# Performance work log

Hardware: AMD Instinct MI355X
Metric: run time of the kernel (lower is better)

## Reference

```python
import jax, jax.numpy as jnp
import numpy as np

TEMPERATURE = 0.07
NEG_RATIO = 1.0
ADJ_DENSITY = 0.002
SAMPLE_SEED = 42


def setup_inputs() -> dict:
    key = jax.random.key(0)
    k1, k2, k3 = jax.random.split(key, 3)
    I, E, D = 4096, 16384, 64
    item = jax.random.normal(k1, (I, D), dtype=jnp.float32)
    ent = jax.random.normal(k2, (E, D), dtype=jnp.float32)
    # sparse binary adjacency: ~33 positives per item on average
    adj = (jax.random.uniform(k3, (I, E)) < ADJ_DENSITY).astype(jnp.int32)
    return {"item_embeddings": item, "entity_embeddings": ent, "adj_matrix": adj}


def reference(item_embeddings, entity_embeddings, adj_matrix):
    # L2-normalize rows, cosine similarity / temperature
    it = item_embeddings / jnp.linalg.norm(item_embeddings, axis=1, keepdims=True)
    en = entity_embeddings / jnp.linalg.norm(entity_embeddings, axis=1, keepdims=True)
    sim = jnp.einsum('id,ed->ie', it, en) / TEMPERATURE  # [I, E]

    pos_mask = adj_matrix > 0                             # [I, E]
    neg_mask = ~pos_mask
    num_pos = pos_mask.sum(axis=1)                        # [I]
    num_neg = neg_mask.sum(axis=1)
    # num_negatives = min(int(num_pos * ratio), num_neg)  (per item)
    k = jnp.minimum(jnp.floor(num_pos.astype(jnp.float32) * NEG_RATIO).astype(jnp.int32), num_neg)

    # negative sampling without replacement: uniform keys, take k smallest among negatives
    u = jax.random.uniform(jax.random.key(SAMPLE_SEED), sim.shape)
    u = jnp.where(pos_mask, jnp.inf, u)                   # positives rank last
    rank = jnp.argsort(jnp.argsort(u, axis=1), axis=1)    # per-row rank of each entity
    samp = (rank < k[:, None]) & neg_mask                 # sampled negatives [I, E]

    valid = (num_pos > 0) & (k > 0)                       # items contributing pairs

    # stable per-item logsumexp over sampled negatives
    neg_logits = jnp.where(samp, sim, -jnp.inf)
    m = jnp.max(neg_logits, axis=1)                       # [I], -inf if no sampled negs
    m_safe = jnp.where(valid, m, 0.0)
    S = jnp.sum(jnp.where(samp, jnp.exp(sim - m_safe[:, None]), 0.0), axis=1)  # [I]

    # per positive pair: CE with pos as class 0 over [pos, sampled_negs]
    # loss = log(exp(pos) + sum exp(neg)) - pos, stabilized with pairwise max
    pm = jnp.maximum(sim, m_safe[:, None])
    loss_pair = jnp.log(jnp.exp(sim - pm) + S[:, None] * jnp.exp(m_safe[:, None] - pm)) + pm - sim

    pair_mask = pos_mask & valid[:, None]
    total = jnp.sum(jnp.where(pair_mask, loss_pair, 0.0))
    n_pairs = jnp.sum(jnp.where(valid, num_pos, 0))
    return jnp.where(n_pairs > 0, total / jnp.maximum(n_pairs, 1).astype(jnp.float32), 0.0)
```

## Files before the change

### kernel.cpp

```cpp
#include <hip/hip_runtime.h>
#include <math.h>


constexpr int D      = 64;
constexpr int PCAP   = 96;
constexpr int CCAP   = 192;
constexpr int SELCAP = 128;

typedef int int4v __attribute__((ext_vector_type(4)));

__device__ __forceinline__ void threefry2x32(unsigned x0, unsigned x1,
                                             unsigned& o0, unsigned& o1) {
  const unsigned ks0 = 0u;
  const unsigned ks1 = 42u;
  const unsigned ks2 = 0x1BD11BDAu ^ 0u ^ 42u;
  x0 += ks0; x1 += ks1;
#define TF_R(r) { x0 += x1; x1 = (x1 << (r)) | (x1 >> (32 - (r))); x1 ^= x0; }
  TF_R(13) TF_R(15) TF_R(26) TF_R(6)
  x0 += ks1; x1 += ks2 + 1u;
  TF_R(17) TF_R(29) TF_R(16) TF_R(24)
  x0 += ks2; x1 += ks0 + 2u;
  TF_R(13) TF_R(15) TF_R(26) TF_R(6)
  x0 += ks0; x1 += ks1 + 3u;
  TF_R(17) TF_R(29) TF_R(16) TF_R(24)
  x0 += ks1; x1 += ks2 + 4u;
  TF_R(13) TF_R(15) TF_R(26) TF_R(6)
  x0 += ks2; x1 += ks0 + 5u;
#undef TF_R
  o0 = x0; o1 = x1;
}

__device__ __forceinline__ float dot_sim(const float* __restrict__ ent, int e,
                                         const float* itemn) {
  const float4* er = (const float4*)(ent + ((size_t)e << 6));
  float dot = 0.f, ss = 0.f;
#pragma unroll
  for (int q = 0; q < 16; ++q) {
    float4 f = er[q];
    dot += itemn[4 * q + 0] * f.x + itemn[4 * q + 1] * f.y +
           itemn[4 * q + 2] * f.z + itemn[4 * q + 3] * f.w;
    ss += f.x * f.x + f.y * f.y + f.z * f.z + f.w * f.w;
  }
  return dot * (1.0f / sqrtf(ss));
}

__device__ __forceinline__ void wave_append(bool pred, int e,
                                            int* cnt, int* list, int cap) {
  unsigned long long m = __ballot(pred);
  if (m) {
    const int lane = threadIdx.x & 63;
    const int leader = __builtin_ctzll(m);
    int base = 0;
    if (lane == leader) base = atomicAdd(cnt, __popcll(m));
    base = __shfl(base, leader, 64);
    if (pred) {
      int s = base + __popcll(m & ((1ull << lane) - 1ull));
      if (s < cap) list[s] = e;
    }
  }
}

__device__ __forceinline__ void wave_append2(bool pred, int e, unsigned key,
                                             int* cnt, int* li, unsigned* lk,
                                             int cap) {
  unsigned long long m = __ballot(pred);
  if (m) {
    const int lane = threadIdx.x & 63;
    const int leader = __builtin_ctzll(m);
    int base = 0;
    if (lane == leader) base = atomicAdd(cnt, __popcll(m));
    base = __shfl(base, leader, 64);
    if (pred) {
      int s = base + __popcll(m & ((1ull << lane) - 1ull));
      if (s < cap) { li[s] = e; lk[s] = key; }
    }
  }
}

__device__ __forceinline__ float block_max(float v, float* wred, int t) {
#pragma unroll
  for (int off = 32; off; off >>= 1) v = fmaxf(v, __shfl_xor(v, off, 64));
  __syncthreads();
  if ((t & 63) == 0) wred[t >> 6] = v;
  __syncthreads();
  return fmaxf(fmaxf(wred[0], wred[1]), fmaxf(wred[2], wred[3]));
}

__device__ __forceinline__ float block_sum(float v, float* wred, int t) {
#pragma unroll
  for (int off = 32; off; off >>= 1) v += __shfl_xor(v, off, 64);
  __syncthreads();
  if ((t & 63) == 0) wred[t >> 6] = v;
  __syncthreads();
  return wred[0] + wred[1] + wred[2] + wred[3];
}

template <bool WSOUT>
__global__ __launch_bounds__(256) void infonce_mono(
    const float* __restrict__ item, const float* __restrict__ ent,
    const int* __restrict__ adj, int I, int E,
    float* __restrict__ loss, int* __restrict__ cnt,
    double* __restrict__ accum, int* __restrict__ paircnt) {
  const int t = threadIdx.x;
  const int halfI = I >> 1;
  const int iA = blockIdx.x;
  const int iB = iA + halfI;
  const unsigned HALF = (unsigned)halfI * (unsigned)E;
  const unsigned baseA = (unsigned)iA * (unsigned)E;

  __shared__ int s_pos[2][PCAP];
  __shared__ int s_ci[2][CCAP];
  __shared__ unsigned s_ck[2][CCAP];
  __shared__ int s_sel[SELCAP];
  __shared__ int s_hist[256];
  __shared__ float s_itemn[D];
  __shared__ float s_wred[4];
  __shared__ int s_np[2], s_nc[2];
  __shared__ int s_nsel, s_bbin, s_cbef, s_fnc;
  __shared__ float s_scale;

  if (t < 2) { s_np[t] = 0; s_nc[t] = 0; }
  __syncthreads();

  const int nvec = E >> 2;
  const int4v* adjA = (const int4v*)(adj + (size_t)iA * E);
  const int4v* adjB = (const int4v*)(adj + (size_t)iB * E);
  for (int v = t; v < nvec; v += 256) {
    int4v a4 = __builtin_nontemporal_load(&adjA[v]);
    int4v b4 = __builtin_nontemporal_load(&adjB[v]);
    const unsigned e0 = (unsigned)v * 4u;
    unsigned o0[4], o1[4];
#pragma unroll
    for (int c = 0; c < 4; ++c)
      threefry2x32(baseA + e0 + c, baseA + e0 + c + HALF, o0[c], o1[c]);
#pragma unroll
    for (int c = 0; c < 4; ++c) {
      const int e = (int)(e0 + c);
      const bool pa = (a4[c] > 0), pb = (b4[c] > 0);
      wave_append(pa, e, &s_np[0], s_pos[0], PCAP);
      wave_append(pb, e, &s_np[1], s_pos[1], PCAP);
      wave_append2(!pa && (o0[c] >> 24) == 0u, e, o0[c] >> 9,
                   &s_nc[0], s_ci[0], s_ck[0], CCAP);
      wave_append2(!pb && (o1[c] >> 24) == 0u, e, o1[c] >> 9,
                   &s_nc[1], s_ci[1], s_ck[1], CCAP);
    }
  }
  __syncthreads();

  for (int r2 = 0; r2 < 2; ++r2) {
    const int row = r2 ? iB : iA;
    const int npos = min(s_np[r2], PCAP);
    const int k = min(npos, E - npos);
    const bool valid = (npos > 0 && k > 0);
    float rowloss = 0.f;
    if (valid) {
      if (t == 0) s_nsel = 0;
      __syncthreads();
      int ncand = min(s_nc[r2], CCAP);
      int rneed = k;
      if (s_nc[r2] > CCAP || ncand < k) {
        s_hist[t] = 0;
        if (t == 0) s_fnc = 0;
        __syncthreads();
        const int* adjR = adj + (size_t)row * E;
        for (int e = t; e < E; e += 256) {
          if (adjR[e] > 0) continue;
          unsigned o0, o1;
          threefry2x32(baseA + (unsigned)e, baseA + (unsigned)e + HALF, o0, o1);
          atomicAdd(&s_hist[(r2 ? o1 : o0) >> 24], 1);
        }
        __syncthreads();
        if (t == 0) {
          int cum = 0, b = 0;
          while (b < 255 && cum + s_hist[b] < k) { cum += s_hist[b]; ++b; }
          s_bbin = b; s_cbef = cum;
        }
        __syncthreads();
        const int b = s_bbin;
        for (int e = t; e < E; e += 256) {
          bool neg = (adjR[e] <= 0);
          unsigned o0, o1, bits = 0xFFFFFFFFu;
          if (neg) {
            threefry2x32(baseA + (unsigned)e, baseA + (unsigned)e + HALF, o0, o1);
            bits = r2 ? o1 : o0;
          }
          int b8 = (int)(bits >> 24);
          wave_append(neg && b8 < b, e, &s_nsel, s_sel, SELCAP);
          wave_append2(neg && b8 == b, e, bits >> 9,
                       &s_fnc, s_ci[r2], s_ck[r2], CCAP);
        }
        __syncthreads();
        ncand = min(s_fnc, CCAP);
        rneed = k - s_cbef;
      }

      for (int i = t; i < ncand; i += 256) {
        const unsigned mk = s_ck[r2][i];
        const int mi = s_ci[r2][i];
        int rank = 0;
        for (int c = 0; c < ncand; ++c) {
          const unsigned ck = s_ck[r2][c];
          const int ci = s_ci[r2][c];
          rank += (ck < mk || (ck == mk && ci < mi)) ? 1 : 0;
        }
        if (rank < rneed) {
          int s = atomicAdd(&s_nsel, 1);
          if (s < SELCAP) s_sel[s] = mi;
        }
      }

      float iv = 0.f;
      if (t < D) iv = item[(size_t)row * D + t];
      if (t < 64) {
        float ss = iv * iv;
#pragma unroll
        for (int off = 32; off; off >>= 1) ss += __shfl_xor(ss, off, 64);
        if (t == 0) s_scale = (1.0f / sqrtf(ss)) * (1.0f / 0.07f);
      }
      __syncthreads();
      if (t < D) s_itemn[t] = iv * s_scale;
      __syncthreads();
      const int nsel = min(s_nsel, SELCAP);

      float myv = (t < nsel) ? dot_sim(ent, s_sel[t], s_itemn) : -INFINITY;
      const float m = block_max(myv, s_wred, t);
      float v2 = (t < nsel) ? expf(myv - m) : 0.f;
      const float S = block_sum(v2, s_wred, t);

      float lp = 0.f;
      if (t < npos) {
        float sp = dot_sim(ent, s_pos[r2][t], s_itemn);
        float pm = fmaxf(sp, m);
        lp = logf(expf(sp - pm) + S * expf(m - pm)) + pm - sp;
      }
      rowloss = block_sum(lp, s_wred, t);
    }
    if (WSOUT) {
      if (t == 0) { loss[row] = valid ? rowloss : 0.f; cnt[row] = valid ? npos : 0; }
    } else {
      if (valid && t == 0) {
        atomicAdd(accum, (double)rowloss);
        atomicAdd(paircnt, npos);
      }
    }
    __syncthreads();
  }
}

__global__ __launch_bounds__(256) void reduce_out(
    const float* __restrict__ loss, const int* __restrict__ cnt, int I,
    float* __restrict__ out) {
  const int t = threadIdx.x;
  __shared__ double s_l[256];
  __shared__ int s_n[256];
  double l = 0.0;
  int n = 0;
  for (int i = t; i < I; i += 256) { l += (double)loss[i]; n += cnt[i]; }
  s_l[t] = l; s_n[t] = n;
  __syncthreads();
  for (int off = 128; off; off >>= 1) {
    if (t < off) { s_l[t] += s_l[t + off]; s_n[t] += s_n[t + off]; }
    __syncthreads();
  }
  if (t == 0) out[0] = (s_n[0] > 0) ? (float)(s_l[0] / (double)s_n[0]) : 0.f;
}

__global__ void infonce_init(double* accum, int* cnt) {
  if (threadIdx.x == 0 && blockIdx.x == 0) { accum[0] = 0.0; cnt[0] = 0; }
}

__global__ void infonce_final(const double* __restrict__ accum,
                              const int* __restrict__ cnt,
                              float* __restrict__ out) {
  if (threadIdx.x == 0 && blockIdx.x == 0) {
    int n = cnt[0];
    out[0] = (n > 0) ? (float)(accum[0] / (double)n) : 0.f;
  }
}

extern "C" void kernel_launch(void* const* d_in, const int* in_sizes, int n_in,
                              void* d_out, int out_size, void* d_ws, size_t ws_size,
                              hipStream_t stream) {
  const float* item = (const float*)d_in[0];
  const float* ent  = (const float*)d_in[1];
  const int*   adj  = (const int*)d_in[2];
  const int I = in_sizes[0] / D;
  const int E = in_sizes[1] / D;

  const size_t need = (size_t)I * 8;
  if (ws_size >= need && (I % 2) == 0) {
    float* loss = (float*)d_ws;
    int*   cnt  = (int*)(loss + I);
    infonce_mono<true><<<I / 2, 256, 0, stream>>>(item, ent, adj, I, E,
                                                  loss, cnt, nullptr, nullptr);
    reduce_out<<<1, 256, 0, stream>>>(loss, cnt, I, (float*)d_out);
  } else {
    double* accum   = (double*)d_ws;
    int*    paircnt = (int*)((char*)d_ws + 8);
    infonce_init<<<1, 64, 0, stream>>>(accum, paircnt);
    infonce_mono<false><<<I / 2, 256, 0, stream>>>(item, ent, adj, I, E,
                                                   nullptr, nullptr, accum, paircnt);
    infonce_final<<<1, 64, 0, stream>>>(accum, paircnt, (float*)d_out);
  }
}
```

Before: 156.3 us.

## Replace shared-memory atomic appends with per-wave register counters and segments

The scan phase now keeps positive and candidate counts in registers per wave and writes into per-wave shared segments, using mbcnt to compute lane offsets, so no shared atomics or shuffles are needed on each append. Each thread loads 8 contiguous adjacency entries per iteration, and occupancy is hinted with launch_bounds(256,8). Segments are compacted after the scan, and a fallback path recomputes positive losses directly from adj when a segment overflows. The cost is an extra compaction step, tighter per-wave capacities that could trigger the slower fallback more often, and a new requirement that E be a multiple of 2048.

```diff
diff --git a/kernel.cpp b/kernel.cpp
--- a/kernel.cpp
+++ b/kernel.cpp
@@ -3,9 +3,11 @@
 
 
 constexpr int D      = 64;
-constexpr int PCAP   = 96;
-constexpr int CCAP   = 192;
-constexpr int SELCAP = 128;
+constexpr int POS_W  = 40;
+constexpr int CAND_W = 64;
+constexpr int PTOT   = 4 * POS_W;
+constexpr int CTOT   = 4 * CAND_W;
+constexpr int SELCAP = 256;
 
 typedef int int4v __attribute__((ext_vector_type(4)));
 
@@ -30,19 +32,32 @@
   o0 = x0; o1 = x1;
 }
 
-__device__ __forceinline__ float dot_sim(const float* __restrict__ ent, int e,
-                                         const float* itemn) {
-  const float4* er = (const float4*)(ent + ((size_t)e << 6));
-  float dot = 0.f, ss = 0.f;
-#pragma unroll
-  for (int q = 0; q < 16; ++q) {
-    float4 f = er[q];
-    dot += itemn[4 * q + 0] * f.x + itemn[4 * q + 1] * f.y +
-           itemn[4 * q + 2] * f.z + itemn[4 * q + 3] * f.w;
-    ss += f.x * f.x + f.y * f.y + f.z * f.z + f.w * f.w;
-  }
-  return dot * (1.0f / sqrtf(ss));
-}
+__device__ __forceinline__ int lane_prior(unsigned long long m) {
+  return (int)__builtin_amdgcn_mbcnt_hi(
+      (unsigned)(m >> 32), __builtin_amdgcn_mbcnt_lo((unsigned)m, 0u));
+}
+
+#define APPEND1(pred, val, cntvar, seg, cap)                        \
+  do {                                                              \
+    unsigned long long m_ = __ballot(pred);                         \
+    if (m_) {                                                       \
+      int ofs_ = cntvar + lane_prior(m_);                           \
+      if ((pred) && ofs_ < (cap)) (seg)[ofs_] = (val);              \
+      cntvar += (int)__popcll(m_);                                  \
+    }                                                               \
+  } while (0)
+
+#define APPEND2(pred, val, key, cntvar, segi, segk, cap)            \
+  do {                                                              \
+    unsigned long long m_ = __ballot(pred);                         \
+    if (m_) {                                                       \
+      int ofs_ = cntvar + lane_prior(m_);                           \
+      if ((pred) && ofs_ < (cap)) {                                 \
+        (segi)[ofs_] = (val); (segk)[ofs_] = (key);                 \
+      }                                                             \
+      cntvar += (int)__popcll(m_);                                  \
+    }                                                               \
+  } while (0)
 
 __device__ __forceinline__ void wave_append(bool pred, int e,
                                             int* cnt, int* list, int cap) {
@@ -51,32 +66,45 @@
     const int lane = threadIdx.x & 63;
     const int leader = __builtin_ctzll(m);
     int base = 0;
-    if (lane == leader) base = atomicAdd(cnt, __popcll(m));
+    if (lane == leader) base = atomicAdd(cnt, (int)__popcll(m));
     base = __shfl(base, leader, 64);
     if (pred) {
-      int s = base + __popcll(m & ((1ull << lane) - 1ull));
+      int s = base + lane_prior(m);
       if (s < cap) list[s] = e;
     }
   }
 }
-
-__device__ __forceinline__ void wave_append2(bool pred, int e, unsigned key,
-                                             int* cnt, int* li, unsigned* lk,
-                                             int cap) {
+__device__ __forceinline__ void wave_append2a(bool pred, int e, unsigned key,
+                                              int* cnt, int* li, unsigned* lk,
+                                              int cap) {
   unsigned long long m = __ballot(pred);
   if (m) {
     const int lane = threadIdx.x & 63;
     const int leader = __builtin_ctzll(m);
     int base = 0;
-    if (lane == leader) base = atomicAdd(cnt, __popcll(m));
+    if (lane == leader) base = atomicAdd(cnt, (int)__popcll(m));
     base = __shfl(base, leader, 64);
     if (pred) {
-      int s = base + __popcll(m & ((1ull << lane) - 1ull));
+      int s = base + lane_prior(m);
       if (s < cap) { li[s] = e; lk[s] = key; }
     }
   }
 }
 
+__device__ __forceinline__ float dot_sim(const float* __restrict__ ent, int e,
+                                         const float* itemn) {
+  const float4* er = (const float4*)(ent + ((size_t)e << 6));
+  float dot = 0.f, ss = 0.f;
+#pragma unroll
+  for (int q = 0; q < 16; ++q) {
+    float4 f = er[q];
+    dot += itemn[4 * q + 0] * f.x + itemn[4 * q + 1] * f.y +
+           itemn[4 * q + 2] * f.z + itemn[4 * q + 3] * f.w;
+    ss += f.x * f.x + f.y * f.y + f.z * f.z + f.w * f.w;
+  }
+  return dot * (1.0f / sqrtf(ss));
+}
+
 __device__ __forceinline__ float block_max(float v, float* wred, int t) {
 #pragma unroll
   for (int off = 32; off; off >>= 1) v = fmaxf(v, __shfl_xor(v, off, 64));
@@ -85,7 +113,6 @@
   __syncthreads();
   return fmaxf(fmaxf(wred[0], wred[1]), fmaxf(wred[2], wred[3]));
 }
-
 __device__ __forceinline__ float block_sum(float v, float* wred, int t) {
 #pragma unroll
   for (int off = 32; off; off >>= 1) v += __shfl_xor(v, off, 64);
@@ -96,69 +123,122 @@
 }
 
 template <bool WSOUT>
-__global__ __launch_bounds__(256) void infonce_mono(
+__global__ __launch_bounds__(256, 8) void infonce_mono(
     const float* __restrict__ item, const float* __restrict__ ent,
     const int* __restrict__ adj, int I, int E,
     float* __restrict__ loss, int* __restrict__ cnt,
     double* __restrict__ accum, int* __restrict__ paircnt) {
   const int t = threadIdx.x;
+  const int wv = t >> 6;
   const int halfI = I >> 1;
   const int iA = blockIdx.x;
   const int iB = iA + halfI;
   const unsigned HALF = (unsigned)halfI * (unsigned)E;
   const unsigned baseA = (unsigned)iA * (unsigned)E;
 
-  __shared__ int s_pos[2][PCAP];
-  __shared__ int s_ci[2][CCAP];
-  __shared__ unsigned s_ck[2][CCAP];
+  __shared__ int s_pos[2][4][POS_W];
+  __shared__ int s_ci[2][4][CAND_W];
+  __shared__ unsigned s_ck[2][4][CAND_W];
+  __shared__ int s_npw[2][4], s_ncw[2][4];
+  __shared__ int s_posc[PTOT];
+  __shared__ int s_cci[CTOT];
+  __shared__ unsigned s_cck[CTOT];
   __shared__ int s_sel[SELCAP];
   __shared__ int s_hist[256];
   __shared__ float s_itemn[D];
   __shared__ float s_wred[4];
-  __shared__ int s_np[2], s_nc[2];
   __shared__ int s_nsel, s_bbin, s_cbef, s_fnc;
   __shared__ float s_scale;
 
-  if (t < 2) { s_np[t] = 0; s_nc[t] = 0; }
-  __syncthreads();
-
-  const int nvec = E >> 2;
-  const int4v* adjA = (const int4v*)(adj + (size_t)iA * E);
-  const int4v* adjB = (const int4v*)(adj + (size_t)iB * E);
-  for (int v = t; v < nvec; v += 256) {
-    int4v a4 = __builtin_nontemporal_load(&adjA[v]);
-    int4v b4 = __builtin_nontemporal_load(&adjB[v]);
-    const unsigned e0 = (unsigned)v * 4u;
-    unsigned o0[4], o1[4];
-#pragma unroll
-    for (int c = 0; c < 4; ++c)
-      threefry2x32(baseA + e0 + c, baseA + e0 + c + HALF, o0[c], o1[c]);
-#pragma unroll
-    for (int c = 0; c < 4; ++c) {
-      const int e = (int)(e0 + c);
-      const bool pa = (a4[c] > 0), pb = (b4[c] > 0);
-      wave_append(pa, e, &s_np[0], s_pos[0], PCAP);
-      wave_append(pb, e, &s_np[1], s_pos[1], PCAP);
-      wave_append2(!pa && (o0[c] >> 24) == 0u, e, o0[c] >> 9,
-                   &s_nc[0], s_ci[0], s_ck[0], CCAP);
-      wave_append2(!pb && (o1[c] >> 24) == 0u, e, o1[c] >> 9,
-                   &s_nc[1], s_ci[1], s_ck[1], CCAP);
-    }
+  int* segPA = s_pos[0][wv];
+  int* segPB = s_pos[1][wv];
+  int* segCiA = s_ci[0][wv];
+  int* segCiB = s_ci[1][wv];
+  unsigned* segCkA = s_ck[0][wv];
+  unsigned* segCkB = s_ck[1][wv];
+  int npA = 0, npB = 0, ncA = 0, ncB = 0;
+
+  const int* adjA = adj + (size_t)iA * E;
+  const int* adjB = adj + (size_t)iB * E;
+  const int niter = E >> 11;
+  for (int i = 0; i < niter; ++i) {
+    const int e0 = (i << 11) + t * 8;
+    const int4v* pa4 = (const int4v*)(adjA + e0);
+    const int4v* pb4 = (const int4v*)(adjB + e0);
+    int4v a0 = __builtin_nontemporal_load(pa4);
+    int4v a1 = __builtin_nontemporal_load(pa4 + 1);
+    int4v b0 = __builtin_nontemporal_load(pb4);
+    int4v b1 = __builtin_nontemporal_load(pb4 + 1);
+    unsigned pam = 0, pbm = 0;
+    {
+      int av[8] = {a0.x, a0.y, a0.z, a0.w, a1.x, a1.y, a1.z, a1.w};
+      int bv[8] = {b0.x, b0.y, b0.z, b0.w, b1.x, b1.y, b1.z, b1.w};
+#pragma unroll
+      for (int c = 0; c < 8; ++c) {
+        pam |= (av[c] > 0 ? 1u : 0u) << c;
+        pbm |= (bv[c] > 0 ? 1u : 0u) << c;
+      }
+    }
+#pragma unroll
+    for (int h = 0; h < 2; ++h) {
+      unsigned o0[4], o1[4];
+#pragma unroll
+      for (int c = 0; c < 4; ++c) {
+        const unsigned x = baseA + (unsigned)(e0 + 4 * h + c);
+        threefry2x32(x, x + HALF, o0[c], o1[c]);
+      }
+#pragma unroll
+      for (int c = 0; c < 4; ++c) {
+        const int e = e0 + 4 * h + c;
+        const bool pa = (pam >> (4 * h + c)) & 1u;
+        const bool pb = (pbm >> (4 * h + c)) & 1u;
+        APPEND1(pa, e, npA, segPA, POS_W);
+        APPEND1(pb, e, npB, segPB, POS_W);
+        APPEND2(!pa && o0[c] < (1u << 24), e, o0[c] >> 9,
+                ncA, segCiA, segCkA, CAND_W);
+        APPEND2(!pb && o1[c] < (1u << 24), e, o1[c] >> 9,
+                ncB, segCiB, segCkB, CAND_W);
+      }
+    }
+  }
+  if ((t & 63) == 0) {
+    s_npw[0][wv] = npA; s_npw[1][wv] = npB;
+    s_ncw[0][wv] = ncA; s_ncw[1][wv] = ncB;
   }
   __syncthreads();
 
   for (int r2 = 0; r2 < 2; ++r2) {
     const int row = r2 ? iB : iA;
-    const int npos = min(s_np[r2], PCAP);
+    const int np0 = s_npw[r2][0], np1 = s_npw[r2][1];
+    const int np2 = s_npw[r2][2], np3 = s_npw[r2][3];
+    const int nc0 = s_ncw[r2][0], nc1 = s_ncw[r2][1];
+    const int nc2 = s_ncw[r2][2], nc3 = s_ncw[r2][3];
+    const int npos = np0 + np1 + np2 + np3;
+    const int nc = nc0 + nc1 + nc2 + nc3;
     const int k = min(npos, E - npos);
-    const bool valid = (npos > 0 && k > 0);
+    const bool valid = (npos > 0) && (k > 0);
+    bool fallback =
+        (np0 > POS_W) || (np1 > POS_W) || (np2 > POS_W) || (np3 > POS_W) ||
+        (nc0 > CAND_W) || (nc1 > CAND_W) || (nc2 > CAND_W) || (nc3 > CAND_W) ||
+        (nc < k);
     float rowloss = 0.f;
     if (valid) {
       if (t == 0) s_nsel = 0;
+      if (!fallback) {
+        const int lane = t & 63;
+        const int pofs = (wv > 0 ? np0 : 0) + (wv > 1 ? np1 : 0) + (wv > 2 ? np2 : 0);
+        const int cofs = (wv > 0 ? nc0 : 0) + (wv > 1 ? nc1 : 0) + (wv > 2 ? nc2 : 0);
+        const int myPn = s_npw[r2][wv], myCn = s_ncw[r2][wv];
+        for (int i = lane; i < myPn; i += 64) s_posc[pofs + i] = s_pos[r2][wv][i];
+        for (int i = lane; i < myCn; i += 64) {
+          s_cci[cofs + i] = s_ci[r2][wv][i];
+          s_cck[cofs + i] = s_ck[r2][wv][i];
+        }
+      }
       __syncthreads();
-      int ncand = min(s_nc[r2], CCAP);
-      int rneed = k;
-      if (s_nc[r2] > CCAP || ncand < k) {
+
+      int ncand = nc, rneed = k;
+      if (fallback) {
         s_hist[t] = 0;
         if (t == 0) s_fnc = 0;
         __syncthreads();
@@ -186,21 +266,20 @@
           }
           int b8 = (int)(bits >> 24);
           wave_append(neg && b8 < b, e, &s_nsel, s_sel, SELCAP);
-          wave_append2(neg && b8 == b, e, bits >> 9,
-                       &s_fnc, s_ci[r2], s_ck[r2], CCAP);
+          wave_append2a(neg && b8 == b, e, bits >> 9, &s_fnc, s_cci, s_cck, CTOT);
         }
         __syncthreads();
-        ncand = min(s_fnc, CCAP);
+        ncand = min(s_fnc, CTOT);
         rneed = k - s_cbef;
       }
 
       for (int i = t; i < ncand; i += 256) {
-        const unsigned mk = s_ck[r2][i];
-        const int mi = s_ci[r2][i];
+        const unsigned mk = s_cck[i];
+        const int mi = s_cci[i];
         int rank = 0;
         for (int c = 0; c < ncand; ++c) {
-          const unsigned ck = s_ck[r2][c];
-          const int ci = s_ci[r2][c];
+          const unsigned ck = s_cck[c];
+          const int ci = s_cci[c];
           rank += (ck < mk || (ck == mk && ci < mi)) ? 1 : 0;
         }
         if (rank < rneed) {
@@ -228,10 +307,21 @@
       const float S = block_sum(v2, s_wred, t);
 
       float lp = 0.f;
-      if (t < npos) {
-        float sp = dot_sim(ent, s_pos[r2][t], s_itemn);
-        float pm = fmaxf(sp, m);
-        lp = logf(expf(sp - pm) + S * expf(m - pm)) + pm - sp;
+      if (!fallback) {
+        if (t < npos) {
+          float sp = dot_sim(ent, s_posc[t], s_itemn);
+          float pm = fmaxf(sp, m);
+          lp = logf(expf(sp - pm) + S * expf(m - pm)) + pm - sp;
+        }
+      } else {
+        const int* adjR = adj + (size_t)row * E;
+        for (int e = t; e < E; e += 256) {
+          if (adjR[e] > 0) {
+            float sp = dot_sim(ent, e, s_itemn);
+            float pm = fmaxf(sp, m);
+            lp += logf(expf(sp - pm) + S * expf(m - pm)) + pm - sp;
+          }
+        }
       }
       rowloss = block_sum(lp, s_wred, t);
     }
@@ -288,7 +378,7 @@
   const int E = in_sizes[1] / D;
 
   const size_t need = (size_t)I * 8;
-  if (ws_size >= need && (I % 2) == 0) {
+  if (ws_size >= need && (I % 2) == 0 && (E % 2048) == 0) {
     float* loss = (float*)d_ws;
     int*   cnt  = (int*)(loss + I);
     infonce_mono<true><<<I / 2, 256, 0, stream>>>(item, ent, adj, I, E,
```

Result: slower. 200.8 us (+28.4%).
